# Kernel tuning notes

Measured on AMD Instinct MI355X. Metric: run time of the kernel, lower is better.

The kernel has to match this reference:

```python
import jax, jax.numpy as jnp
import numpy as np

act = jax.nn.softplus

def _lin(h, W, b):
    return h @ W + b

def _residual_stack(h, Ws, bs):
    # Ws: [L,2,D,D], bs: [L,2,D]; Residual: x + Lin(act(Lin(act(x))))
    for i in range(Ws.shape[0]):
        t = _lin(act(h), Ws[i, 0], bs[i, 0])
        t = _lin(act(t), Ws[i, 1], bs[i, 1])
        h = t + h
    return h

def setup_inputs() -> dict:
    key = jax.random.key(0)
    N, E, D, R = 40000, 640000, 128, 64
    n_int, n_atomic, n_out = 2, 2, 1
    ks = jax.random.split(key, 24)
    s = 1.0 / np.sqrt(D)
    sr = 1.0 / np.sqrt(R)
    inp = {
        'x': jax.random.normal(ks[0], (N, D), jnp.float32),
        'g_ij': jax.random.uniform(ks[1], (E, R), jnp.float32),
        'idx_i': jax.random.randint(ks[2], (E,), 0, N, jnp.int32),
        'idx_j': jax.random.randint(ks[3], (E,), 0, N, jnp.int32),
        'n_atoms': N,
        'u': jax.random.uniform(ks[4], (D,), jnp.float32),  # torch.rand(n_atom_basis)
        'W_g': jax.random.normal(ks[5], (R, D), jnp.float32) * sr,
        'b_g': jnp.zeros((D,), jnp.float32),
        'W_j': jax.random.normal(ks[6], (D, D), jnp.float32) * s,
        'b_j': jnp.zeros((D,), jnp.float32),
        'W_i': jax.random.normal(ks[7], (D, D), jnp.float32) * s,
        'b_i': jnp.zeros((D,), jnp.float32),
        'W_f': jax.random.normal(ks[8], (D, D), jnp.float32) * s,
        'b_f': jnp.zeros((D,), jnp.float32),
        'Wres_int': jax.random.normal(ks[9], (n_int, 2, D, D), jnp.float32) * s,
        'bres_int': jnp.zeros((n_int, 2, D), jnp.float32),
        'Wres_atom': jax.random.normal(ks[10], (n_atomic, 2, D, D), jnp.float32) * s,
        'bres_atom': jnp.zeros((n_atomic, 2, D), jnp.float32),
        'Wres_out': jax.random.normal(ks[11], (n_out, 2, D, D), jnp.float32) * s,
        'bres_out': jnp.zeros((n_out, 2, D), jnp.float32),
        'W_out': jax.random.normal(ks[12], (D, D), jnp.float32) * s,
        'b_out': jnp.zeros((D,), jnp.float32),
    }
    return inp

def reference(x, g_ij, idx_i, idx_j, n_atoms, u,
              W_g, b_g, W_j, b_j, W_i, b_i, W_f, b_f,
              Wres_int, bres_int, Wres_atom, bres_atom,
              Wres_out, bres_out, W_out, b_out):
    # --- PhysNetInteraction ---
    x_j = x[idx_j]                                   # [E,D] gather
    xp = u * x                                       # random feature scale
    vp = act(_lin(act(x_j), W_j, b_j)) * _lin(g_ij, W_g, b_g)   # [E,D]
    vm = act(_lin(act(x), W_i, b_i))                 # [N,D]
    v = jax.ops.segment_sum(vp, idx_i, num_segments=n_atoms) + vm
    v = _residual_stack(v, Wres_int, bres_int)
    v = act(v)
    h = xp + _lin(v, W_f, b_f)
    # --- atomic residuals ---
    h = _residual_stack(h, Wres_atom, bres_atom)
    # --- Output block ---
    o = _residual_stack(h, Wres_out, bres_out)
    o = _lin(act(o), W_out, b_out)
    return (o, h)
```

## Files before the change

kernel.cpp:

```cpp
#include <hip/hip_runtime.h>


#define D 128
#define TILE 64
#define TILE2 128
#define LDP 136
#define SLOT 16384
#define EPB 64

typedef __attribute__((ext_vector_type(8))) short s8v;
typedef __attribute__((ext_vector_type(4))) unsigned short us4;
typedef __attribute__((ext_vector_type(4))) float f32x4;

struct Frag { f32x4 v[8]; };
struct WReg { s8v w[4]; };

__device__ __forceinline__ float sp_act(float x) {
    float t = __builtin_amdgcn_exp2f(-fabsf(x) * 1.44269504088896f);
    return fmaxf(x, 0.f) + 0.69314718055994f * __builtin_amdgcn_logf(1.0f + t);
}
__device__ __forceinline__ unsigned short f2bf(float f) {
    unsigned int u = __float_as_uint(f);
    u += 0x7fffu + ((u >> 16) & 1u);
    return (unsigned short)(u >> 16);
}
__device__ __forceinline__ float bf2f(unsigned short h) {
    return __uint_as_float(((unsigned int)h) << 16);
}

__global__ void prep_weights(
    const float* __restrict__ Wj, const float* __restrict__ Wi,
    const float* __restrict__ Wf, const float* __restrict__ Wout,
    const float* __restrict__ Wri, const float* __restrict__ Wra,
    const float* __restrict__ Wro, const float* __restrict__ Wg,
    unsigned short* __restrict__ wt)
{
    int id = blockIdx.x;
    const float* src;
    int K = D;
    if      (id == 0)  src = Wj;
    else if (id == 1)  src = Wi;
    else if (id == 2)  src = Wf;
    else if (id == 3)  src = Wout;
    else if (id < 8)   src = Wri + (id - 4) * D * D;
    else if (id < 12)  src = Wra + (id - 8) * D * D;
    else if (id < 14)  src = Wro + (id - 12) * D * D;
    else             { src = Wg; K = 64; }
    unsigned short* dst = wt + id * SLOT;
    int total = K * D;
    for (int e = threadIdx.x; e < total; e += blockDim.x) {
        int k = e >> 7, n = e & 127;
        dst[n * K + k] = f2bf(src[e]);
    }
}

template <int NT>
__device__ __forceinline__ void load_w128(const unsigned short* __restrict__ wt,
                                          unsigned short (*Wl)[LDP], int t) {
#pragma unroll
    for (int q = 0; q < 2048 / NT; ++q) {
        int c = t + q * NT;
        int row = c >> 4;
        int k = (c & 15) * 8;
        *(s8v*)&Wl[row][k] = *(const s8v*)(wt + row * 128 + k);
    }
}

__device__ __forceinline__ void mm128(const unsigned short (*Ax)[LDP],
                                      const unsigned short (*Wl)[LDP],
                                      int wrow, int lane, Frag& acc) {
    int r = lane & 15, g4 = lane >> 4;
#pragma unroll
    for (int k0 = 0; k0 < 4; ++k0) {
        s8v a = *(const s8v*)&Ax[wrow + r][k0 * 32 + g4 * 8];
#pragma unroll
        for (int n = 0; n < 8; ++n) {
            s8v b = *(const s8v*)&Wl[n * 16 + r][k0 * 32 + g4 * 8];
            acc.v[n] = __builtin_amdgcn_mfma_f32_16x16x32_bf16(a, b, acc.v[n], 0, 0, 0);
        }
    }
}

__global__ __launch_bounds__(256) void node_pre(
    const float* __restrict__ x, const unsigned short* __restrict__ wt,
    const float* __restrict__ bj, const float* __restrict__ bi,
    unsigned short* __restrict__ P, float* __restrict__ v, int N)
{
    __shared__ __align__(16) unsigned short Ax[TILE][LDP];
    __shared__ __align__(16) unsigned short Wl[D][LDP];
    int t = threadIdx.x;
    int r0 = blockIdx.x * TILE;
#pragma unroll
    for (int q = 0; q < 8; ++q) {
        int c = t + q * 256;
        int row = c >> 5;
        int col = (c & 31) * 4;
        int gr = r0 + row;
        f32x4 xv = {0.f, 0.f, 0.f, 0.f};
        if (gr < N) xv = *(const f32x4*)(x + (size_t)gr * D + col);
        us4 w = { f2bf(sp_act(xv[0])), f2bf(sp_act(xv[1])),
                  f2bf(sp_act(xv[2])), f2bf(sp_act(xv[3])) };
        *(us4*)&Ax[row][col] = w;
    }
    load_w128<256>(wt + 0 * SLOT, Wl, t);
    s8v wreg0, wreg1, wreg2, wreg3, wreg4, wreg5, wreg6, wreg7;
    {
        const unsigned short* wsrc = wt + 1 * SLOT;
        int row = t >> 4, k = (t & 15) * 8;
        wreg0 = *(const s8v*)(wsrc + (row +   0) * 128 + k);
        wreg1 = *(const s8v*)(wsrc + (row +  16) * 128 + k);
        wreg2 = *(const s8v*)(wsrc + (row +  32) * 128 + k);
        wreg3 = *(const s8v*)(wsrc + (row +  48) * 128 + k);
        wreg4 = *(const s8v*)(wsrc + (row +  64) * 128 + k);
        wreg5 = *(const s8v*)(wsrc + (row +  80) * 128 + k);
        wreg6 = *(const s8v*)(wsrc + (row +  96) * 128 + k);
        wreg7 = *(const s8v*)(wsrc + (row + 112) * 128 + k);
    }
    __syncthreads();

    int lane = t & 63, wv = t >> 6, wrow = wv * 16;
    int r = lane & 15, g4 = lane >> 4;
    Frag acc;
#pragma unroll
    for (int n = 0; n < 8; ++n) { float b = bj[n * 16 + r]; acc.v[n] = (f32x4){b, b, b, b}; }
    mm128(Ax, Wl, wrow, lane, acc);
#pragma unroll
    for (int i = 0; i < 4; ++i) {
        int row = r0 + wrow + g4 * 4 + i;
        if (row < N) {
            s8v p;
#pragma unroll
            for (int n = 0; n < 8; ++n) p[n] = (short)f2bf(sp_act(acc.v[n][i]));
            __builtin_nontemporal_store(p, (s8v*)(P + (size_t)row * D + r * 8));
        }
    }
    __syncthreads();
    {
        int row = t >> 4, k = (t & 15) * 8;
        *(s8v*)&Wl[row +   0][k] = wreg0;
        *(s8v*)&Wl[row +  16][k] = wreg1;
        *(s8v*)&Wl[row +  32][k] = wreg2;
        *(s8v*)&Wl[row +  48][k] = wreg3;
        *(s8v*)&Wl[row +  64][k] = wreg4;
        *(s8v*)&Wl[row +  80][k] = wreg5;
        *(s8v*)&Wl[row +  96][k] = wreg6;
        *(s8v*)&Wl[row + 112][k] = wreg7;
    }
    __syncthreads();
#pragma unroll
    for (int n = 0; n < 8; ++n) { float b = bi[n * 16 + r]; acc.v[n] = (f32x4){b, b, b, b}; }
    mm128(Ax, Wl, wrow, lane, acc);
#pragma unroll
    for (int i = 0; i < 4; ++i) {
        int row = r0 + wrow + g4 * 4 + i;
        if (row < N) {
            f32x4 lo, hi;
#pragma unroll
            for (int n = 0; n < 4; ++n) {
                lo[n] = sp_act(acc.v[n][i]);
                hi[n] = sp_act(acc.v[n + 4][i]);
            }
            __builtin_nontemporal_store(lo, (f32x4*)(v + (size_t)row * D + r * 8));
            __builtin_nontemporal_store(hi, (f32x4*)(v + (size_t)row * D + r * 8 + 4));
        }
    }
}

__global__ void zero_ints(int* __restrict__ a, int n) {
    int i = blockIdx.x * blockDim.x + threadIdx.x;
    if (i < n) a[i] = 0;
}
__global__ void hist_kernel(const int* __restrict__ idx_i, int* __restrict__ counts, int E) {
    for (int e = blockIdx.x * blockDim.x + threadIdx.x; e < E; e += gridDim.x * blockDim.x)
        atomicAdd(&counts[idx_i[e]], 1);
}
__global__ __launch_bounds__(1024) void scan_kernel(const int* __restrict__ counts,
                                                    int* __restrict__ offsets, int n) {
    __shared__ int wsum[16];
    int t = threadIdx.x, lane = t & 63, w = t >> 6;
    int carry = 0;
    for (int base = 0; base < n; base += 1024) {
        int i = base + t;
        int val = (i < n) ? counts[i] : 0;
        int s = val;
#pragma unroll
        for (int d = 1; d < 64; d <<= 1) {
            int y = __shfl_up(s, d, 64);
            if (lane >= d) s += y;
        }
        if (lane == 63) wsum[w] = s;
        __syncthreads();
        if (w == 0) {
            int ws = (lane < 16) ? wsum[lane] : 0;
#pragma unroll
            for (int d = 1; d < 16; d <<= 1) {
                int y = __shfl_up(ws, d, 64);
                if (lane >= d) ws += y;
            }
            if (lane < 16) wsum[lane] = ws;
        }
        __syncthreads();
        int wpre = (w == 0) ? 0 : wsum[w - 1];
        if (i < n) offsets[i] = carry + wpre + (s - val);
        int total = wsum[15];
        __syncthreads();
        carry += total;
    }
}
__global__ void scatter_kernel(const int* __restrict__ idx_i,
                               const int* __restrict__ offsets,
                               int* __restrict__ cursor, int* __restrict__ perm, int E) {
    for (int e = blockIdx.x * blockDim.x + threadIdx.x; e < E; e += gridDim.x * blockDim.x) {
        int i = idx_i[e];
        int p = offsets[i] + atomicAdd(&cursor[i], 1);
        perm[p] = e;
    }
}

__global__ __launch_bounds__(256) void edge_gather(
    const float* __restrict__ g, const int* __restrict__ idx_i,
    const int* __restrict__ idx_j, const int* __restrict__ perm,
    const unsigned short* __restrict__ wtg, const float* __restrict__ bg,
    const unsigned short* __restrict__ P, float* __restrict__ v, int E)
{
    __shared__ __align__(16) unsigned char smem[33792];
    __shared__ int s_pe[EPB], s_ni[EPB], s_nj[EPB];
    unsigned short (*Gx)[72] = (unsigned short(*)[72])smem;
    unsigned short (*WG)[72] = (unsigned short(*)[72])(smem + 9216);
    float (*Vx)[132] = (float(*)[132])smem;

    int t = threadIdx.x;
    int e0 = blockIdx.x * EPB;
    if (t < EPB) {
        int e = e0 + t;
        if (e < E) {
            int pe = perm[e];
            s_pe[t] = pe;
            s_ni[t] = idx_i[pe];
            s_nj[t] = idx_j[pe];
        } else {
            s_pe[t] = -1; s_ni[t] = -1; s_nj[t] = 0;
        }
    }
    __syncthreads();
#pragma unroll
    for (int q = 0; q < 4; ++q) {
        int c = t + q * 256;
        int row = c >> 4;
        int col = (c & 15) * 4;
        int pe = s_pe[row];
        f32x4 gv = {0.f, 0.f, 0.f, 0.f};
        if (pe >= 0)
            gv = __builtin_nontemporal_load((const f32x4*)(g + (size_t)pe * 64 + col));
        us4 w = { f2bf(gv[0]), f2bf(gv[1]), f2bf(gv[2]), f2bf(gv[3]) };
        *(us4*)&Gx[row][col] = w;
    }
#pragma unroll
    for (int q = 0; q < 4; ++q) {
        int c = t + q * 256;
        int row = c >> 3;
        int k = (c & 7) * 8;
        *(s8v*)&WG[row][k] = *(const s8v*)(wtg + row * 64 + k);
    }
    __syncthreads();
    int lane = t & 63, wv = t >> 6;
    int r = lane & 15, g4 = lane >> 4;
    Frag acc;
#pragma unroll
    for (int n = 0; n < 8; ++n) { float b = bg[n * 16 + r]; acc.v[n] = (f32x4){b, b, b, b}; }
#pragma unroll
    for (int k0 = 0; k0 < 2; ++k0) {
        s8v a = *(const s8v*)&Gx[wv * 16 + r][k0 * 32 + g4 * 8];
#pragma unroll
        for (int n = 0; n < 8; ++n) {
            s8v b = *(const s8v*)&WG[n * 16 + r][k0 * 32 + g4 * 8];
            acc.v[n] = __builtin_amdgcn_mfma_f32_16x16x32_bf16(a, b, acc.v[n], 0, 0, 0);
        }
    }
    __syncthreads();
#pragma unroll
    for (int i = 0; i < 4; ++i) {
        int el = wv * 16 + g4 * 4 + i;
        bool valid = (e0 + el) < E;
        s8v pv = *(const s8v*)(P + (size_t)s_nj[el] * D + r * 8);
        f32x4 lo, hi;
#pragma unroll
        for (int n = 0; n < 4; ++n) {
            lo[n] = valid ? acc.v[n][i]     * bf2f((unsigned short)pv[n])     : 0.f;
            hi[n] = valid ? acc.v[n + 4][i] * bf2f((unsigned short)pv[n + 4]) : 0.f;
        }
        *(f32x4*)&Vx[el][r * 8]     = lo;
        *(f32x4*)&Vx[el][r * 8 + 4] = hi;
    }
    __syncthreads();
    int f = t & 127, half = t >> 7;
    int estart = half * 32;
    int ecap = E - e0; if (ecap > EPB) ecap = EPB;
    int eend = estart + 32; if (eend > ecap) eend = ecap;
    if (estart < eend) {
        float accv = 0.f;
        int cur = s_ni[estart];
        for (int e = estart; e < eend; ++e) {
            int node = s_ni[e];
            if (node != cur) {
                unsafeAtomicAdd(v + (size_t)cur * D + f, accv);
                accv = 0.f; cur = node;
            }
            accv += Vx[e][f];
        }
        unsafeAtomicAdd(v + (size_t)cur * D + f, accv);
    }
}

__device__ __forceinline__ void stage_w(WReg& wr,
                                        const unsigned short* __restrict__ wtp, int t) {
#pragma unroll
    for (int q = 0; q < 4; ++q) {
        int c = t + q * 512; int row = c >> 4; int k = (c & 15) * 8;
        wr.w[q] = *(const s8v*)(wtp + row * 128 + k);
    }
}

template <bool RESID>
__device__ __forceinline__ Frag do_layer(
    const Frag in, const Frag resid,
    const float* __restrict__ bias,
    WReg& wreg, const unsigned short* __restrict__ next_wt,
    unsigned short (*Ax)[LDP], unsigned short (*Wl)[LDP],
    int t, int lane, int wrow, int r, int g4)
{
    __syncthreads();
#pragma unroll
    for (int n = 0; n < 8; ++n)
#pragma unroll
        for (int i = 0; i < 4; ++i)
            Ax[wrow + g4 * 4 + i][n * 16 + r] = f2bf(sp_act(in.v[n][i]));
#pragma unroll
    for (int q = 0; q < 4; ++q) {
        int c = t + q * 512; int row = c >> 4; int k = (c & 15) * 8;
        *(s8v*)&Wl[row][k] = wreg.w[q];
    }
    if (next_wt) stage_w(wreg, next_wt, t);
    __syncthreads();
    Frag out;
#pragma unroll
    for (int n = 0; n < 8; ++n) {
        float b = bias[n * 16 + r];
        f32x4 bb = {b, b, b, b};
        out.v[n] = RESID ? bb + resid.v[n] : bb;
    }
    mm128(Ax, Wl, wrow, lane, out);
    return out;
}

__device__ __forceinline__ void store_tile(
    const Frag val, float* __restrict__ dst, int r0, int N,
    float (*St)[132], int t, int wv, int r, int g4)
{
#pragma unroll
    for (int half = 0; half < 2; ++half) {
        __syncthreads();
        if ((wv >> 2) == half) {
            int lr = (wv & 3) * 16 + g4 * 4;
#pragma unroll
            for (int n = 0; n < 8; ++n)
#pragma unroll
                for (int i = 0; i < 4; ++i)
                    St[lr + i][n * 16 + r] = val.v[n][i];
        }
        __syncthreads();
#pragma unroll
        for (int q = 0; q < 4; ++q) {
            int idx = t + q * 512;
            int row = idx >> 5, c4 = (idx & 31) * 4;
            int gr = r0 + half * 64 + row;
            if (gr < N) {
                f32x4 vv = *(const f32x4*)&St[row][c4];
                __builtin_nontemporal_store(vv, (f32x4*)(dst + (size_t)gr * D + c4));
            }
        }
    }
}

__global__ __launch_bounds__(512) void phaseB(
    const float* __restrict__ vin, const float* __restrict__ x,
    const float* __restrict__ u, const unsigned short* __restrict__ wt,
    const float* __restrict__ bri, const float* __restrict__ bra,
    const float* __restrict__ bro, const float* __restrict__ bfv,
    const float* __restrict__ bout,
    float* __restrict__ o_out, float* __restrict__ h_out, int N)
{
    __shared__ __align__(16) unsigned short Ax[TILE2][LDP];
    __shared__ __align__(16) unsigned short Wl[D][LDP];
    float (*St)[132] = (float(*)[132])Wl;
    int t = threadIdx.x, lane = t & 63, wv = t >> 6, wrow = wv * 16;
    int r = lane & 15, g4 = lane >> 4;
    int r0 = blockIdx.x * TILE2;

    WReg wreg;
    stage_w(wreg, wt + 4 * SLOT, t);

    Frag h;
#pragma unroll
    for (int i = 0; i < 4; ++i) {
        int row = r0 + wrow + g4 * 4 + i;
        f32x4 lo = {0.f, 0.f, 0.f, 0.f}, hi = {0.f, 0.f, 0.f, 0.f};
        if (row < N) {
            lo = __builtin_nontemporal_load((const f32x4*)(vin + (size_t)row * D + r * 8));
            hi = __builtin_nontemporal_load((const f32x4*)(vin + (size_t)row * D + r * 8 + 4));
        }
#pragma unroll
        for (int n = 0; n < 4; ++n) { h.v[n][i] = lo[n]; h.v[n + 4][i] = hi[n]; }
    }

    Frag t0;
    t0 = do_layer<false>(h,  h, bri + 0 * D, wreg, wt +  5 * SLOT, Ax, Wl, t, lane, wrow, r, g4);
    h  = do_layer<true >(t0, h, bri + 1 * D, wreg, wt +  6 * SLOT, Ax, Wl, t, lane, wrow, r, g4);
    t0 = do_layer<false>(h,  h, bri + 2 * D, wreg, wt +  7 * SLOT, Ax, Wl, t, lane, wrow, r, g4);
    h  = do_layer<true >(t0, h, bri + 3 * D, wreg, wt +  2 * SLOT, Ax, Wl, t, lane, wrow, r, g4);
    Frag ux;
#pragma unroll
    for (int n = 0; n < 8; ++n)
#pragma unroll
        for (int i = 0; i < 4; ++i) {
            int row = r0 + wrow + g4 * 4 + i;
            float xv = (row < N) ? x[(size_t)row * D + n * 16 + r] : 0.f;
            ux.v[n][i] = u[n * 16 + r] * xv;
        }
    h  = do_layer<true >(h,  ux, bfv, wreg, wt + 8 * SLOT, Ax, Wl, t, lane, wrow, r, g4);
    t0 = do_layer<false>(h,  h, bra + 0 * D, wreg, wt +  9 * SLOT, Ax, Wl, t, lane, wrow, r, g4);
    h  = do_layer<true >(t0, h, bra + 1 * D, wreg, wt + 10 * SLOT, Ax, Wl, t, lane, wrow, r, g4);
    t0 = do_layer<false>(h,  h, bra + 2 * D, wreg, wt + 11 * SLOT, Ax, Wl, t, lane, wrow, r, g4);
    h  = do_layer<true >(t0, h, bra + 3 * D, wreg, wt + 12 * SLOT, Ax, Wl, t, lane, wrow, r, g4);
    store_tile(h, h_out, r0, N, St, t, wv, r, g4);
    t0 = do_layer<false>(h,  h, bro + 0 * D, wreg, wt + 13 * SLOT, Ax, Wl, t, lane, wrow, r, g4);
    h  = do_layer<true >(t0, h, bro + 1 * D, wreg, wt +  3 * SLOT, Ax, Wl, t, lane, wrow, r, g4);
    t0 = do_layer<false>(h,  h, bout,        wreg, nullptr,        Ax, Wl, t, lane, wrow, r, g4);
    store_tile(t0, o_out, r0, N, St, t, wv, r, g4);
}

extern "C" void kernel_launch(void* const* d_in, const int* in_sizes, int n_in,
                              void* d_out, int out_size, void* d_ws, size_t ws_size,
                              hipStream_t stream)
{
    const float* x     = (const float*)d_in[0];
    const float* g     = (const float*)d_in[1];
    const int*   idx_i = (const int*)d_in[2];
    const int*   idx_j = (const int*)d_in[3];
    const float* u     = (const float*)d_in[5];
    const float* Wg    = (const float*)d_in[6];
    const float* bg    = (const float*)d_in[7];
    const float* Wj    = (const float*)d_in[8];
    const float* bj    = (const float*)d_in[9];
    const float* Wi    = (const float*)d_in[10];
    const float* bi    = (const float*)d_in[11];
    const float* Wf    = (const float*)d_in[12];
    const float* bf    = (const float*)d_in[13];
    const float* Wri   = (const float*)d_in[14];
    const float* bri   = (const float*)d_in[15];
    const float* Wra   = (const float*)d_in[16];
    const float* bra   = (const float*)d_in[17];
    const float* Wro   = (const float*)d_in[18];
    const float* bro   = (const float*)d_in[19];
    const float* Wout  = (const float*)d_in[20];
    const float* bout  = (const float*)d_in[21];

    int N = in_sizes[0] / D;
    int E = in_sizes[2];

    float* out = (float*)d_out;
    float* v     = out;
    float* h_out = out + (size_t)N * D;
    unsigned short* P = (unsigned short*)h_out;
    unsigned short* wt = (unsigned short*)d_ws;

    int* ibase   = (int*)(out + (size_t)N * D + (size_t)N * D / 2);
    int* counts  = ibase;
    int* offsets = ibase + N;
    int* cursor  = ibase + 2 * (size_t)N;
    int* perm    = ibase + 3 * (size_t)N;

    prep_weights<<<15, 256, 0, stream>>>(Wj, Wi, Wf, Wout, Wri, Wra, Wro, Wg, wt);

    int nb = (N + TILE - 1) / TILE;
    node_pre<<<nb, 256, 0, stream>>>(x, wt, bj, bi, P, v, N);

    zero_ints<<<(3 * N + 255) / 256, 256, 0, stream>>>(ibase, 3 * N);
    hist_kernel<<<1024, 256, 0, stream>>>(idx_i, counts, E);
    scan_kernel<<<1, 1024, 0, stream>>>(counts, offsets, N);
    scatter_kernel<<<1024, 256, 0, stream>>>(idx_i, offsets, cursor, perm, E);

    int eb = (E + EPB - 1) / EPB;
    edge_gather<<<eb, 256, 0, stream>>>(g, idx_i, idx_j, perm, wt + 14 * SLOT, bg,
                                        P, v, E);

    int nb2 = (N + TILE2 - 1) / TILE2;
    phaseB<<<nb2, 512, 0, stream>>>(v, x, u, wt, bri, bra, bro, bf, bout,
                                    out, h_out, N);
}
```

Before: 315.1 us.

## Presort edge indices in scatter and load edge features straight into registers

The scatter pass now writes idx_i and idx_j in sorted order next to perm, so the edge kernel reads contiguous arrays instead of doing dependent perm→idx gathers. The edge kernel loads each lane's g row fragment directly into registers, converts it to bf16 for MFMA without staging in LDS, and issues the P gathers early so they overlap the weight staging and the matmul. The cost is two extra scatter writes per edge, the extra index arrays in scratch space past perm, and higher register pressure. The g loads also become ordinary loads instead of nontemporal ones.

New measurement: 324.0 us, median of 2. 2.8% more time.

```diff
diff --git a/kernel.cpp b/kernel.cpp
--- a/kernel.cpp
+++ b/kernel.cpp
@@ -208,52 +208,61 @@
     }
 }
 __global__ void scatter_kernel(const int* __restrict__ idx_i,
+                               const int* __restrict__ idx_j,
                                const int* __restrict__ offsets,
-                               int* __restrict__ cursor, int* __restrict__ perm, int E) {
+                               int* __restrict__ cursor, int* __restrict__ perm,
+                               int* __restrict__ sni, int* __restrict__ snj, int E) {
     for (int e = blockIdx.x * blockDim.x + threadIdx.x; e < E; e += gridDim.x * blockDim.x) {
         int i = idx_i[e];
         int p = offsets[i] + atomicAdd(&cursor[i], 1);
         perm[p] = e;
+        sni[p] = i;
+        snj[p] = idx_j[e];
     }
 }
 
 __global__ __launch_bounds__(256) void edge_gather(
-    const float* __restrict__ g, const int* __restrict__ idx_i,
-    const int* __restrict__ idx_j, const int* __restrict__ perm,
+    const float* __restrict__ g, const int* __restrict__ spe,
+    const int* __restrict__ sni, const int* __restrict__ snj,
     const unsigned short* __restrict__ wtg, const float* __restrict__ bg,
     const unsigned short* __restrict__ P, float* __restrict__ v, int E)
 {
     __shared__ __align__(16) unsigned char smem[33792];
-    __shared__ int s_pe[EPB], s_ni[EPB], s_nj[EPB];
-    unsigned short (*Gx)[72] = (unsigned short(*)[72])smem;
-    unsigned short (*WG)[72] = (unsigned short(*)[72])(smem + 9216);
+    __shared__ int s_ni[EPB];
+    unsigned short (*WG)[72] = (unsigned short(*)[72])smem;
     float (*Vx)[132] = (float(*)[132])smem;
 
     int t = threadIdx.x;
     int e0 = blockIdx.x * EPB;
+    int lane = t & 63, wv = t >> 6;
+    int r = lane & 15, g4 = lane >> 4;
+
     if (t < EPB) {
         int e = e0 + t;
-        if (e < E) {
-            int pe = perm[e];
-            s_pe[t] = pe;
-            s_ni[t] = idx_i[pe];
-            s_nj[t] = idx_j[pe];
-        } else {
-            s_pe[t] = -1; s_ni[t] = -1; s_nj[t] = 0;
-        }
-    }
-    __syncthreads();
-#pragma unroll
-    for (int q = 0; q < 4; ++q) {
-        int c = t + q * 256;
-        int row = c >> 4;
-        int col = (c & 15) * 4;
-        int pe = s_pe[row];
-        f32x4 gv = {0.f, 0.f, 0.f, 0.f};
-        if (pe >= 0)
-            gv = __builtin_nontemporal_load((const f32x4*)(g + (size_t)pe * 64 + col));
-        us4 w = { f2bf(gv[0]), f2bf(gv[1]), f2bf(gv[2]), f2bf(gv[3]) };
-        *(us4*)&Gx[row][col] = w;
+        s_ni[t] = (e < E) ? sni[e] : -1;
+    }
+
+    int myedge = e0 + wv * 16 + r;
+    int mype = (myedge < E) ? spe[myedge] : 0;
+    f32x4 glo0, ghi0, glo1, ghi1;
+    {
+        const float* gp = g + (size_t)mype * 64 + g4 * 8;
+        glo0 = *(const f32x4*)(gp);
+        ghi0 = *(const f32x4*)(gp + 4);
+        glo1 = *(const f32x4*)(gp + 32);
+        ghi1 = *(const f32x4*)(gp + 36);
+    }
+    s8v pv0, pv1, pv2, pv3;
+    {
+        int eb = e0 + wv * 16 + g4 * 4;
+        int nj0 = (eb + 0 < E) ? snj[eb + 0] : 0;
+        int nj1 = (eb + 1 < E) ? snj[eb + 1] : 0;
+        int nj2 = (eb + 2 < E) ? snj[eb + 2] : 0;
+        int nj3 = (eb + 3 < E) ? snj[eb + 3] : 0;
+        pv0 = *(const s8v*)(P + (size_t)nj0 * D + r * 8);
+        pv1 = *(const s8v*)(P + (size_t)nj1 * D + r * 8);
+        pv2 = *(const s8v*)(P + (size_t)nj2 * D + r * 8);
+        pv3 = *(const s8v*)(P + (size_t)nj3 * D + r * 8);
     }
 #pragma unroll
     for (int q = 0; q < 4; ++q) {
@@ -263,36 +272,48 @@
         *(s8v*)&WG[row][k] = *(const s8v*)(wtg + row * 64 + k);
     }
     __syncthreads();
-    int lane = t & 63, wv = t >> 6;
-    int r = lane & 15, g4 = lane >> 4;
+
     Frag acc;
 #pragma unroll
     for (int n = 0; n < 8; ++n) { float b = bg[n * 16 + r]; acc.v[n] = (f32x4){b, b, b, b}; }
-#pragma unroll
-    for (int k0 = 0; k0 < 2; ++k0) {
-        s8v a = *(const s8v*)&Gx[wv * 16 + r][k0 * 32 + g4 * 8];
+    {
+        s8v a0, a1;
+#pragma unroll
+        for (int j = 0; j < 4; ++j) {
+            a0[j]     = (short)f2bf(glo0[j]);
+            a0[j + 4] = (short)f2bf(ghi0[j]);
+            a1[j]     = (short)f2bf(glo1[j]);
+            a1[j + 4] = (short)f2bf(ghi1[j]);
+        }
 #pragma unroll
         for (int n = 0; n < 8; ++n) {
-            s8v b = *(const s8v*)&WG[n * 16 + r][k0 * 32 + g4 * 8];
-            acc.v[n] = __builtin_amdgcn_mfma_f32_16x16x32_bf16(a, b, acc.v[n], 0, 0, 0);
-        }
-    }
-    __syncthreads();
+            s8v b = *(const s8v*)&WG[n * 16 + r][0 * 32 + g4 * 8];
+            acc.v[n] = __builtin_amdgcn_mfma_f32_16x16x32_bf16(a0, b, acc.v[n], 0, 0, 0);
+        }
+#pragma unroll
+        for (int n = 0; n < 8; ++n) {
+            s8v b = *(const s8v*)&WG[n * 16 + r][1 * 32 + g4 * 8];
+            acc.v[n] = __builtin_amdgcn_mfma_f32_16x16x32_bf16(a1, b, acc.v[n], 0, 0, 0);
+        }
+    }
+    __syncthreads();
+
 #pragma unroll
     for (int i = 0; i < 4; ++i) {
         int el = wv * 16 + g4 * 4 + i;
         bool valid = (e0 + el) < E;
-        s8v pv = *(const s8v*)(P + (size_t)s_nj[el] * D + r * 8);
+        s8v pvv = (i == 0) ? pv0 : (i == 1) ? pv1 : (i == 2) ? pv2 : pv3;
         f32x4 lo, hi;
 #pragma unroll
         for (int n = 0; n < 4; ++n) {
-            lo[n] = valid ? acc.v[n][i]     * bf2f((unsigned short)pv[n])     : 0.f;
-            hi[n] = valid ? acc.v[n + 4][i] * bf2f((unsigned short)pv[n + 4]) : 0.f;
+            lo[n] = valid ? acc.v[n][i]     * bf2f((unsigned short)pvv[n])     : 0.f;
+            hi[n] = valid ? acc.v[n + 4][i] * bf2f((unsigned short)pvv[n + 4]) : 0.f;
         }
         *(f32x4*)&Vx[el][r * 8]     = lo;
         *(f32x4*)&Vx[el][r * 8 + 4] = hi;
     }
     __syncthreads();
+
     int f = t & 127, half = t >> 7;
     int estart = half * 32;
     int ecap = E - e0; if (ecap > EPB) ecap = EPB;
@@ -479,6 +500,8 @@
     int* offsets = ibase + N;
     int* cursor  = ibase + 2 * (size_t)N;
     int* perm    = ibase + 3 * (size_t)N;
+    int* sni     = perm + E;
+    int* snj     = sni + E;
 
     prep_weights<<<15, 256, 0, stream>>>(Wj, Wi, Wf, Wout, Wri, Wra, Wro, Wg, wt);
 
@@ -488,10 +511,11 @@
     zero_ints<<<(3 * N + 255) / 256, 256, 0, stream>>>(ibase, 3 * N);
     hist_kernel<<<1024, 256, 0, stream>>>(idx_i, counts, E);
     scan_kernel<<<1, 1024, 0, stream>>>(counts, offsets, N);
-    scatter_kernel<<<1024, 256, 0, stream>>>(idx_i, offsets, cursor, perm, E);
+    scatter_kernel<<<1024, 256, 0, stream>>>(idx_i, idx_j, offsets, cursor,
+                                             perm, sni, snj, E);
 
     int eb = (E + EPB - 1) / EPB;
-    edge_gather<<<eb, 256, 0, stream>>>(g, idx_i, idx_j, perm, wt + 14 * SLOT, bg,
+    edge_gather<<<eb, 256, 0, stream>>>(g, perm, sni, snj, wt + 14 * SLOT, bg,
                                         P, v, E);
 
     int nb2 = (N + TILE2 - 1) / TILE2;
```
